# Kernel tuning notes

Measured on AMD Instinct MI355X. Metric: run time of the kernel, lower is better.

The kernel has to match this reference:

```python
import jax, jax.numpy as jnp
import numpy as np

B, L, D = 8, 64, 768
F, P, A = 50, 49, 49   # frames, patches, attention dim
N, C = 20000, 36       # grid points, grid_size**2 cells
LN_EPS = 1e-12


def setup_inputs() -> dict:
    key = jax.random.key(0)
    ks = jax.random.split(key, 16)
    s = 0.02
    return {
        "lang": jax.random.normal(ks[0], (B, L, D), jnp.float32),
        "lang_cls": jax.random.normal(ks[1], (B, A), jnp.float32),
        "frames": jax.random.normal(ks[2], (B, F, P, A), jnp.float32),
        "candidates": jax.random.normal(ks[3], (B, C, 2), jnp.float32),
        "grid_fts": jax.random.normal(ks[4], (B, N, D), jnp.float32),
        "grid_index": jax.random.randint(ks[5], (B, N), 0, C, jnp.int32),
        # SoftDotAttention params (bias=False in torch)
        "W_in": jax.random.normal(ks[6], (A, A), jnp.float32) * s,
        "W_out": jax.random.normal(ks[7], (A, 2 * A), jnp.float32) * s,
        # fc2: 49 -> demb
        "W_fc2": jax.random.normal(ks[8], (D, A), jnp.float32) * s,
        "b_fc2": jnp.zeros((D,), jnp.float32),
        # text_proj / grid_proj: 768 -> 768
        "W_text": jax.random.normal(ks[9], (D, D), jnp.float32) * s,
        "b_text": jnp.zeros((D,), jnp.float32),
        "W_grid": jax.random.normal(ks[10], (D, D), jnp.float32) * s,
        "b_grid": jnp.zeros((D,), jnp.float32),
        # candidate_encoder: Linear(2, demb) + LayerNorm(demb)
        "W_cand": jax.random.normal(ks[11], (D, 2), jnp.float32) * s,
        "b_cand": jnp.zeros((D,), jnp.float32),
        "ln_g": jnp.ones((D,), jnp.float32),
        "ln_b": jnp.zeros((D,), jnp.float32),
    }


def reference(lang, lang_cls, frames, candidates, grid_fts, grid_index,
              W_in, W_out, W_fc2, b_fc2, W_text, b_text, W_grid, b_grid,
              W_cand, b_cand, ln_g, ln_b):
    # ---- SoftDotAttention over every frame (vectorized over F) ----
    target = lang_cls @ W_in.T                                  # [B,A]
    attn = jnp.einsum('bfpa,ba->bfp', frames, target)           # [B,F,P]
    attn = jax.nn.softmax(attn, axis=-1)
    wctx = jnp.einsum('bfp,bfpa->bfa', attn, frames)            # [B,F,A]
    h = jnp.broadcast_to(lang_cls[:, None, :], wctx.shape)      # [B,F,A]
    att_frame = jnp.tanh(jnp.concatenate([wctx, h], -1) @ W_out.T)  # [B,F,A]
    emb_frames = att_frame @ W_fc2.T + b_fc2                    # [B,F,D]

    # ---- grid segment softmax-reduce ----
    text = lang @ W_text.T + b_text                             # [B,L,D]
    # score of each grid point = max over language tokens
    w = jnp.einsum('bnd,bld->bnl', grid_fts, text).max(-1)      # [B,N]
    g = grid_fts @ W_grid.T + b_grid                            # [B,N,D]
    mask = grid_index[..., None] == jnp.arange(C)[None, None]   # [B,N,C]
    logits = jnp.where(mask, w[..., None], -jnp.inf)            # [B,N,C]
    m = logits.max(axis=1, keepdims=True)                       # [B,1,C]
    m = jnp.where(jnp.isfinite(m), m, 0.0)
    e = jnp.where(mask, jnp.exp(logits - m), 0.0)
    den = e.sum(axis=1, keepdims=True)                          # [B,1,C]
    p = jnp.where(den > 0, e / jnp.maximum(den, 1e-30), 0.0)    # [B,N,C]
    grid_map = jnp.einsum('bnc,bnd->bcd', p, g)                 # [B,C,D]

    # ---- candidate encoder: Linear + LayerNorm, scaled by lang[:, :1, :] ----
    c = candidates @ W_cand.T + b_cand                          # [B,C,D]
    mu = c.mean(-1, keepdims=True)
    var = ((c - mu) ** 2).mean(-1, keepdims=True)
    c = (c - mu) * jax.lax.rsqrt(var + LN_EPS) * ln_g + ln_b
    emb_cand = c * lang[:, :1, :] + grid_map                    # [B,C,D]

    return jnp.concatenate([emb_frames, emb_cand], axis=1)      # [B,F+C,D]
```

## Files before the change

kernel.cpp:

```cpp
#include <hip/hip_runtime.h>
#include <math.h>

#define Bh 8
#define Lh 64
#define Dh 768
#define Fh 50
#define Ph 49
#define Ah 49
#define Nh 20000
#define Ch 36
#define CAP 2048
#define NCH 8
#define CUTE 2e-6f

typedef __bf16 bf16x8 __attribute__((ext_vector_type(8)));
typedef float f32x4 __attribute__((ext_vector_type(4)));
union U { uint4 u; bf16x8 v; };

__device__ __forceinline__ void cvt2(float a0, float a1, unsigned& h, unsigned& l) {
    unsigned u0 = __float_as_uint(a0), u1 = __float_as_uint(a1);
    unsigned h0 = u0 & 0xFFFF0000u, h1 = u1 & 0xFFFF0000u;
    h = (h0 >> 16) | h1;
    float l0 = a0 - __uint_as_float(h0);
    float l1 = a1 - __uint_as_float(h1);
    l = (__float_as_uint(l0) >> 16) | (__float_as_uint(l1) & 0xFFFF0000u);
}

__device__ __forceinline__ void cvt8(float4 p, float4 q, bf16x8& h8, bf16x8& l8) {
    U h, l;
    cvt2(p.x, p.y, h.u.x, l.u.x);
    cvt2(p.z, p.w, h.u.y, l.u.y);
    cvt2(q.x, q.y, h.u.z, l.u.z);
    cvt2(q.z, q.w, h.u.w, l.u.w);
    h8 = h.v; l8 = l.v;
}

__device__ __forceinline__ float dec_max(unsigned u) {
    if (u == 0u) return 0.f;
    return (u & 0x80000000u) ? __uint_as_float(u ^ 0x80000000u) : __uint_as_float(~u);
}

__global__ __launch_bounds__(256) void k_setup(const float* __restrict__ lang,
                                               const float* __restrict__ Wt,
                                               const float* __restrict__ bt,
                                               const float* __restrict__ frames,
                                               const float* __restrict__ lang_cls,
                                               const float* __restrict__ W_in,
                                               const float* __restrict__ W_out,
                                               const float* __restrict__ W_fc2,
                                               const float* __restrict__ b_fc2,
                                               uint4* __restrict__ textH,
                                               uint4* __restrict__ textL,
                                               unsigned* __restrict__ m_u,
                                               float* __restrict__ den,
                                               int* __restrict__ cnt,
                                               float* __restrict__ out) {
    __shared__ float smem[8 * Dh];
    int bx = blockIdx.x;
    int tid = threadIdx.x;

    if (bx < 64) {
        int b  = bx >> 3;
        int l0 = (bx & 7) * 8;
        float* ls = smem;
        for (int i = tid; i < 8 * Dh; i += 256)
            ls[i] = lang[((size_t)(b * Lh + l0 + i / Dh)) * Dh + (i % Dh)];
        __syncthreads();
        float acc[8][3];
#pragma unroll
        for (int li = 0; li < 8; ++li)
#pragma unroll
            for (int j = 0; j < 3; ++j) acc[li][j] = 0.f;
        for (int k = 0; k < Dh; k += 4) {
            float4 v[8];
#pragma unroll
            for (int li = 0; li < 8; ++li) v[li] = *(const float4*)&ls[li * Dh + k];
#pragma unroll
            for (int j = 0; j < 3; ++j) {
                int d = tid + j * 256;
                float4 wv = *(const float4*)&Wt[(size_t)d * Dh + k];
#pragma unroll
                for (int li = 0; li < 8; ++li)
                    acc[li][j] += wv.x * v[li].x + wv.y * v[li].y
                                + wv.z * v[li].z + wv.w * v[li].w;
            }
        }
        __syncthreads();
#pragma unroll
        for (int li = 0; li < 8; ++li)
#pragma unroll
            for (int j = 0; j < 3; ++j) {
                int d = tid + j * 256;
                ls[li * Dh + d] = acc[li][j] + bt[d];
            }
        __syncthreads();
        for (int i = tid; i < 768; i += 256) {
            int li = i / 96, idx = i % 96, ks = idx >> 2, j = idx & 3;
            int col = l0 + li, ct = col >> 4;
            const float* src = ls + li * Dh + ks * 32 + j * 8;
            U h, lo;
            cvt2(src[0], src[1], h.u.x, lo.u.x);
            cvt2(src[2], src[3], h.u.y, lo.u.y);
            cvt2(src[4], src[5], h.u.z, lo.u.z);
            cvt2(src[6], src[7], h.u.w, lo.u.w);
            int gid = ((b * 24 + ks) * 4 + ct) * 64 + (col & 15) + 16 * j;
            textH[gid] = h.u;
            textL[gid] = lo.u;
        }
    } else if (bx < 464) {
        int fid = bx - 64;
        int b = fid / Fh, f = fid % Fh;
        float* fr = smem;
        float* tg = smem + 2401;
        float* cl = smem + 2450;
        float* at = smem + 2499;
        float* wc = smem + 2548;
        float* af = smem + 2597;
        const float* fp = frames + ((size_t)(b * Fh + f)) * (Ph * Ah);
        for (int i = tid; i < Ph * Ah; i += 256) fr[i] = fp[i];
        if (tid < Ah) {
            cl[tid] = lang_cls[b * Ah + tid];
            float s = 0.f;
            for (int k = 0; k < Ah; ++k) s += lang_cls[b * Ah + k] * W_in[tid * Ah + k];
            tg[tid] = s;
        }
        __syncthreads();
        if (tid < Ph) {
            float s = 0.f;
            for (int a = 0; a < Ah; ++a) s += fr[tid * Ah + a] * tg[a];
            at[tid] = s;
        }
        __syncthreads();
        if (tid < 64) {
            float raw = (tid < Ph) ? at[tid] : -3.4e38f;
            float v = raw;
            for (int m = 32; m; m >>= 1) v = fmaxf(v, __shfl_xor(v, m));
            float e = (tid < Ph) ? expf(raw - v) : 0.f;
            float s = e;
            for (int m = 32; m; m >>= 1) s += __shfl_xor(s, m);
            if (tid < Ph) at[tid] = e / s;
        }
        __syncthreads();
        if (tid < Ah) {
            float s = 0.f;
            for (int p = 0; p < Ph; ++p) s += at[p] * fr[p * Ah + tid];
            wc[tid] = s;
        }
        __syncthreads();
        if (tid < Ah) {
            float s = 0.f;
            for (int a = 0; a < Ah; ++a)
                s += wc[a] * W_out[tid * (2 * Ah) + a] + cl[a] * W_out[tid * (2 * Ah) + Ah + a];
            af[tid] = tanhf(s);
        }
        __syncthreads();
        for (int d = tid; d < Dh; d += 256) {
            float s = b_fc2[d];
            for (int j = 0; j < Ah; ++j) s += af[j] * W_fc2[d * Ah + j];
            out[((size_t)(b * (Fh + Ch) + f)) * Dh + d] = s;
        }
    } else {
        for (int i = tid; i < Bh * Ch; i += 256) { m_u[i] = 0u; den[i] = 0.f; cnt[i] = 0; }
    }
}

__global__ __launch_bounds__(256) void k_wgf(const float* __restrict__ Wg,
                                             uint4* __restrict__ WgH,
                                             uint4* __restrict__ WgL) {
    int gid = blockIdx.x * 256 + threadIdx.x;
    int l = gid & 63;
    int rest = gid >> 6;
    int ct = rest % 48, ks = rest / 48;
    const float* src = Wg + (size_t)(ct * 16 + (l & 15)) * Dh + ks * 32 + (l >> 4) * 8;
    float4 p = *(const float4*)src;
    float4 q = *(const float4*)(src + 4);
    U h, lo;
    cvt2(p.x, p.y, h.u.x, lo.u.x);
    cvt2(p.z, p.w, h.u.y, lo.u.y);
    cvt2(q.x, q.y, h.u.z, lo.u.z);
    cvt2(q.z, q.w, h.u.w, lo.u.w);
    WgH[gid] = h.u;
    WgL[gid] = lo.u;
}

__global__ __launch_bounds__(256) void k_w(const float* __restrict__ grid,
                                           const uint4* __restrict__ textH,
                                           const uint4* __restrict__ textL,
                                           const int* __restrict__ gi,
                                           float* __restrict__ w,
                                           unsigned* __restrict__ m_u) {
    __shared__ float lds[2][4096];
    __shared__ unsigned mu[Ch];
    int b = blockIdx.y;
    int tid = threadIdx.x;
    int wv = tid >> 6, l = tid & 63;
    int n0 = blockIdx.x * 128;
    if (tid < Ch) mu[tid] = 0u;

    const float* gb = grid + (size_t)b * Nh * Dh;
    const uint4* pbh = textH + (size_t)b * 6144 + l;
    const uint4* pbl = textL + (size_t)b * 6144 + l;

    const float* srcA[4]; int dA[4];
#pragma unroll
    for (int r = 0; r < 4; ++r) {
        int s = r * 256 + tid, row = s >> 3, pos = s & 7;
        int rowg = n0 + row; if (rowg >= Nh) rowg = Nh - 1;
        srcA[r] = gb + (size_t)rowg * Dh + pos * 4;
        dA[r] = row * 32 + ((pos ^ (row & 7)) << 2);
    }
    int lm = l & 15, lh = l >> 4, r7 = lm & 7;
    int oA[2][2];
#pragma unroll
    for (int rt = 0; rt < 2; ++rt)
#pragma unroll
        for (int j = 0; j < 2; ++j)
            oA[rt][j] = (wv * 32 + rt * 16 + lm) * 32 + (((lh * 2 + j) ^ r7) << 2);

    {
        float4 v0 = *(const float4*)srcA[0];
        float4 v1 = *(const float4*)srcA[1];
        float4 v2 = *(const float4*)srcA[2];
        float4 v3 = *(const float4*)srcA[3];
        *(float4*)&lds[0][dA[0]] = v0;
        *(float4*)&lds[0][dA[1]] = v1;
        *(float4*)&lds[0][dA[2]] = v2;
        *(float4*)&lds[0][dA[3]] = v3;
    }
    __syncthreads();

    f32x4 acc[2][4];
#pragma unroll
    for (int i = 0; i < 2; ++i)
#pragma unroll
        for (int j = 0; j < 4; ++j) acc[i][j] = (f32x4){0.f, 0.f, 0.f, 0.f};

    for (int t = 0; t < 24; ++t) {
        int cur = t & 1;
        float4 p0, p1, p2, p3;
        bool pf = (t < 23);
        if (pf) {
            int o = (t + 1) * 32;
            p0 = *(const float4*)(srcA[0] + o);
            p1 = *(const float4*)(srcA[1] + o);
            p2 = *(const float4*)(srcA[2] + o);
            p3 = *(const float4*)(srcA[3] + o);
        }
        uint4 bh0 = pbh[t * 256 +   0], bh1 = pbh[t * 256 +  64];
        uint4 bh2 = pbh[t * 256 + 128], bh3 = pbh[t * 256 + 192];
        uint4 bl0 = pbl[t * 256 +   0], bl1 = pbl[t * 256 +  64];
        uint4 bl2 = pbl[t * 256 + 128], bl3 = pbl[t * 256 + 192];

        const float* L = lds[cur];
        float4 a00 = *(const float4*)&L[oA[0][0]];
        float4 a01 = *(const float4*)&L[oA[0][1]];
        float4 a10 = *(const float4*)&L[oA[1][0]];
        float4 a11 = *(const float4*)&L[oA[1][1]];
        bf16x8 ah0, al0, ah1, al1;
        cvt8(a00, a01, ah0, al0);
        cvt8(a10, a11, ah1, al1);

        uint4 bhu[4] = {bh0, bh1, bh2, bh3};
        uint4 blu[4] = {bl0, bl1, bl2, bl3};
#pragma unroll
        for (int ct = 0; ct < 4; ++ct) {
            U ubh, ubl; ubh.u = bhu[ct]; ubl.u = blu[ct];
            bf16x8 bh = ubh.v, bl = ubl.v;
            acc[0][ct] = __builtin_amdgcn_mfma_f32_16x16x32_bf16(ah0, bh, acc[0][ct], 0, 0, 0);
            acc[0][ct] = __builtin_amdgcn_mfma_f32_16x16x32_bf16(al0, bh, acc[0][ct], 0, 0, 0);
            acc[0][ct] = __builtin_amdgcn_mfma_f32_16x16x32_bf16(ah0, bl, acc[0][ct], 0, 0, 0);
            acc[1][ct] = __builtin_amdgcn_mfma_f32_16x16x32_bf16(ah1, bh, acc[1][ct], 0, 0, 0);
            acc[1][ct] = __builtin_amdgcn_mfma_f32_16x16x32_bf16(al1, bh, acc[1][ct], 0, 0, 0);
            acc[1][ct] = __builtin_amdgcn_mfma_f32_16x16x32_bf16(ah1, bl, acc[1][ct], 0, 0, 0);
        }
        if (pf) {
            float* D = lds[cur ^ 1];
            *(float4*)&D[dA[0]] = p0;
            *(float4*)&D[dA[1]] = p1;
            *(float4*)&D[dA[2]] = p2;
            *(float4*)&D[dA[3]] = p3;
        }
        __syncthreads();
    }

#pragma unroll
    for (int rt = 0; rt < 2; ++rt) {
        float m[4];
#pragma unroll
        for (int r = 0; r < 4; ++r) {
            m[r] = fmaxf(fmaxf(acc[rt][0][r], acc[rt][1][r]),
                         fmaxf(acc[rt][2][r], acc[rt][3][r]));
            m[r] = fmaxf(m[r], __shfl_xor(m[r], 1));
            m[r] = fmaxf(m[r], __shfl_xor(m[r], 2));
            m[r] = fmaxf(m[r], __shfl_xor(m[r], 4));
            m[r] = fmaxf(m[r], __shfl_xor(m[r], 8));
        }
        if (lm == 0) {
#pragma unroll
            for (int r = 0; r < 4; ++r) {
                int row = n0 + wv * 32 + rt * 16 + lh * 4 + r;
                if (row < Nh) {
                    w[b * Nh + row] = m[r];
                    unsigned u = __float_as_uint(m[r]);
                    u = (u & 0x80000000u) ? ~u : (u | 0x80000000u);
                    atomicMax(&mu[gi[b * Nh + row]], u);
                }
            }
        }
    }
    __syncthreads();
    if (tid < Ch && mu[tid]) atomicMax(&m_u[b * Ch + tid], mu[tid]);
}

__global__ __launch_bounds__(256) void k_epc(const float* __restrict__ w,
                                             const int* __restrict__ gi,
                                             const unsigned* __restrict__ m_u,
                                             float* __restrict__ den,
                                             int* __restrict__ cnt,
                                             int* __restrict__ bn,
                                             float* __restrict__ bp) {
    int b = blockIdx.y;
    int n = blockIdx.x * 256 + threadIdx.x;
    __shared__ float dn[Ch];
    if (threadIdx.x < Ch) dn[threadIdx.x] = 0.f;
    __syncthreads();
    if (n < Nh) {
        int c = gi[b * Nh + n];
        float e = expf(w[b * Nh + n] - dec_max(m_u[b * Ch + c]));
        atomicAdd(&dn[c], e);
        if (e > CUTE) {
            int pos = atomicAdd(&cnt[b * Ch + c], 1);
            if (pos < CAP) {
                bn[(b * Ch + c) * CAP + pos] = n;
                bp[(b * Ch + c) * CAP + pos] = e;
            }
        }
    }
    __syncthreads();
    if (threadIdx.x < Ch && dn[threadIdx.x] != 0.f)
        atomicAdd(&den[b * Ch + threadIdx.x], dn[threadIdx.x]);
}

__global__ __launch_bounds__(256) void k_S3(const float* __restrict__ grid,
                                            const int* __restrict__ cnt,
                                            const int* __restrict__ bn,
                                            const float* __restrict__ bp,
                                            float* __restrict__ Spart) {
    int c = blockIdx.x, dq = blockIdx.y;
    int b = blockIdx.z >> 3, ch = blockIdx.z & 7;
    int d = dq * 256 + threadIdx.x;
    int len = cnt[b * Ch + c]; if (len > CAP) len = CAP;
    int i0 = ch * (CAP / NCH);
    int i1 = i0 + (CAP / NCH); if (i1 > len) i1 = len;
    size_t base = (size_t)(b * Ch + c) * CAP;
    size_t po = ((size_t)(b * Ch + c) * NCH + ch) * Dh + d;
    const float* gb = grid + (size_t)b * Nh * Dh + d;
    float a[8] = {0.f, 0.f, 0.f, 0.f, 0.f, 0.f, 0.f, 0.f};
    int i = i0;
    for (; i + 8 <= i1; i += 8) {
        int nn[8]; float pp[8];
#pragma unroll
        for (int j = 0; j < 8; ++j) { nn[j] = bn[base + i + j]; pp[j] = bp[base + i + j]; }
#pragma unroll
        for (int j = 0; j < 8; ++j) a[j] += pp[j] * gb[(size_t)nn[j] * Dh];
    }
    for (; i < i1; ++i) a[0] += bp[base + i] * gb[(size_t)bn[base + i] * Dh];
    Spart[po] = ((a[0] + a[1]) + (a[2] + a[3])) + ((a[4] + a[5]) + (a[6] + a[7]));
}

__global__ __launch_bounds__(256) void k_red(const float* __restrict__ Spart,
                                             float* __restrict__ S) {
    int bc = blockIdx.x, dq = blockIdx.y;
    int d = dq * 256 + threadIdx.x;
    float s = 0.f;
#pragma unroll
    for (int ch = 0; ch < NCH; ++ch)
        s += Spart[((size_t)bc * NCH + ch) * Dh + d];
    S[(size_t)bc * Dh + d] = s;
}

__global__ __launch_bounds__(256) void k_gg2(const float* __restrict__ S,
                                             const float* __restrict__ den,
                                             const uint4* __restrict__ WgH,
                                             const uint4* __restrict__ WgL,
                                             const float* __restrict__ bg,
                                             float* __restrict__ G) {
    __shared__ float lds[2][4096];
    int tid = threadIdx.x;
    int wv = tid >> 6, l = tid & 63;
    int m0 = blockIdx.y * 128;
    int dt = blockIdx.x;

    const uint4* pbh = WgH + (size_t)dt * 256 + l;
    const uint4* pbl = WgL + (size_t)dt * 256 + l;

    const float* srcA[4]; int dA[4];
#pragma unroll
    for (int r = 0; r < 4; ++r) {
        int s = r * 256 + tid, row = s >> 3, pos = s & 7;
        int rowg = m0 + row; if (rowg >= Bh * Ch) rowg = Bh * Ch - 1;
        srcA[r] = S + (size_t)rowg * Dh + pos * 4;
        dA[r] = row * 32 + ((pos ^ (row & 7)) << 2);
    }
    int lm = l & 15, lh = l >> 4, r7 = lm & 7;
    int oA[2][2];
#pragma unroll
    for (int rt = 0; rt < 2; ++rt)
#pragma unroll
        for (int j = 0; j < 2; ++j)
            oA[rt][j] = (wv * 32 + rt * 16 + lm) * 32 + (((lh * 2 + j) ^ r7) << 2);

    {
        float4 v0 = *(const float4*)srcA[0];
        float4 v1 = *(const float4*)srcA[1];
        float4 v2 = *(const float4*)srcA[2];
        float4 v3 = *(const float4*)srcA[3];
        *(float4*)&lds[0][dA[0]] = v0;
        *(float4*)&lds[0][dA[1]] = v1;
        *(float4*)&lds[0][dA[2]] = v2;
        *(float4*)&lds[0][dA[3]] = v3;
    }
    __syncthreads();

    f32x4 acc[2][4];
#pragma unroll
    for (int i = 0; i < 2; ++i)
#pragma unroll
        for (int j = 0; j < 4; ++j) acc[i][j] = (f32x4){0.f, 0.f, 0.f, 0.f};

    for (int t = 0; t < 24; ++t) {
        int cur = t & 1;
        float4 p0, p1, p2, p3;
        bool pf = (t < 23);
        if (pf) {
            int o = (t + 1) * 32;
            p0 = *(const float4*)(srcA[0] + o);
            p1 = *(const float4*)(srcA[1] + o);
            p2 = *(const float4*)(srcA[2] + o);
            p3 = *(const float4*)(srcA[3] + o);
        }
        uint4 bh0 = pbh[t * 3072 +   0], bh1 = pbh[t * 3072 +  64];
        uint4 bh2 = pbh[t * 3072 + 128], bh3 = pbh[t * 3072 + 192];
        uint4 bl0 = pbl[t * 3072 +   0], bl1 = pbl[t * 3072 +  64];
        uint4 bl2 = pbl[t * 3072 + 128], bl3 = pbl[t * 3072 + 192];

        const float* L = lds[cur];
        float4 a00 = *(const float4*)&L[oA[0][0]];
        float4 a01 = *(const float4*)&L[oA[0][1]];
        float4 a10 = *(const float4*)&L[oA[1][0]];
        float4 a11 = *(const float4*)&L[oA[1][1]];
        bf16x8 ah0, al0, ah1, al1;
        cvt8(a00, a01, ah0, al0);
        cvt8(a10, a11, ah1, al1);

        uint4 bhu[4] = {bh0, bh1, bh2, bh3};
        uint4 blu[4] = {bl0, bl1, bl2, bl3};
#pragma unroll
        for (int ct = 0; ct < 4; ++ct) {
            U ubh, ubl; ubh.u = bhu[ct]; ubl.u = blu[ct];
            bf16x8 bh = ubh.v, bl = ubl.v;
            acc[0][ct] = __builtin_amdgcn_mfma_f32_16x16x32_bf16(ah0, bh, acc[0][ct], 0, 0, 0);
            acc[0][ct] = __builtin_amdgcn_mfma_f32_16x16x32_bf16(al0, bh, acc[0][ct], 0, 0, 0);
            acc[0][ct] = __builtin_amdgcn_mfma_f32_16x16x32_bf16(ah0, bl, acc[0][ct], 0, 0, 0);
            acc[1][ct] = __builtin_amdgcn_mfma_f32_16x16x32_bf16(ah1, bh, acc[1][ct], 0, 0, 0);
            acc[1][ct] = __builtin_amdgcn_mfma_f32_16x16x32_bf16(al1, bh, acc[1][ct], 0, 0, 0);
            acc[1][ct] = __builtin_amdgcn_mfma_f32_16x16x32_bf16(ah1, bl, acc[1][ct], 0, 0, 0);
        }
        if (pf) {
            float* D = lds[cur ^ 1];
            *(float4*)&D[dA[0]] = p0;
            *(float4*)&D[dA[1]] = p1;
            *(float4*)&D[dA[2]] = p2;
            *(float4*)&D[dA[3]] = p3;
        }
        __syncthreads();
    }

#pragma unroll
    for (int rt = 0; rt < 2; ++rt) {
#pragma unroll
        for (int r = 0; r < 4; ++r) {
            int row = m0 + wv * 32 + rt * 16 + lh * 4 + r;
            if (row < Bh * Ch) {
                float dv = den[row];
                float inv = (dv > 0.f) ? 1.f / dv : 0.f;
#pragma unroll
                for (int ct = 0; ct < 4; ++ct) {
                    int d = dt * 64 + ct * 16 + lm;
                    G[(size_t)row * Dh + d] = acc[rt][ct][r] * inv + bg[d];
                }
            }
        }
    }
}

__global__ __launch_bounds__(256) void k_final(const float* __restrict__ G,
                                               const float* __restrict__ den,
                                               const float* __restrict__ cands,
                                               const float* __restrict__ W_cand,
                                               const float* __restrict__ b_cand,
                                               const float* __restrict__ ln_g,
                                               const float* __restrict__ ln_b,
                                               const float* __restrict__ lang,
                                               float* __restrict__ out) {
    int b = blockIdx.x / Ch, c = blockIdx.x % Ch;
    int tid = threadIdx.x;
    __shared__ float cv[Dh];
    __shared__ float red[8];
    __shared__ float mu_s, rs_s;
    float cx = cands[(b * Ch + c) * 2 + 0], cy = cands[(b * Ch + c) * 2 + 1];
    for (int d = tid; d < Dh; d += 256)
        cv[d] = W_cand[d * 2] * cx + W_cand[d * 2 + 1] * cy + b_cand[d];
    __syncthreads();
    float ls = 0.f;
    for (int d = tid; d < Dh; d += 256) ls += cv[d];
    for (int m = 32; m; m >>= 1) ls += __shfl_xor(ls, m);
    if ((tid & 63) == 0) red[tid >> 6] = ls;
    __syncthreads();
    if (tid == 0) mu_s = (red[0] + red[1] + red[2] + red[3]) * (1.f / Dh);
    __syncthreads();
    float mu = mu_s;
    float lv = 0.f;
    for (int d = tid; d < Dh; d += 256) { float t = cv[d] - mu; lv += t * t; }
    for (int m = 32; m; m >>= 1) lv += __shfl_xor(lv, m);
    if ((tid & 63) == 0) red[4 + (tid >> 6)] = lv;
    __syncthreads();
    if (tid == 0) rs_s = rsqrtf((red[4] + red[5] + red[6] + red[7]) * (1.f / Dh) + 1e-12f);
    __syncthreads();
    float rs = rs_s;
    float dv = den[b * Ch + c];
#pragma unroll
    for (int j = 0; j < 3; ++j) {
        int d = tid + j * 256;
        float gm = (dv > 0.f) ? G[(size_t)(b * Ch + c) * Dh + d] : 0.f;
        float cn = (cv[d] - mu) * rs * ln_g[d] + ln_b[d];
        out[((size_t)(b * (Fh + Ch) + Fh + c)) * Dh + d] =
            cn * lang[((size_t)b * Lh) * Dh + d] + gm;
    }
}

extern "C" void kernel_launch(void* const* d_in, const int* in_sizes, int n_in,
                              void* d_out, int out_size, void* d_ws, size_t ws_size,
                              hipStream_t stream) {
    (void)in_sizes; (void)n_in; (void)out_size; (void)ws_size;
    const float* lang      = (const float*)d_in[0];
    const float* lang_cls  = (const float*)d_in[1];
    const float* frames    = (const float*)d_in[2];
    const float* cands     = (const float*)d_in[3];
    const float* grid_fts  = (const float*)d_in[4];
    const int*   grid_idx  = (const int*)d_in[5];
    const float* W_in      = (const float*)d_in[6];
    const float* W_out     = (const float*)d_in[7];
    const float* W_fc2     = (const float*)d_in[8];
    const float* b_fc2     = (const float*)d_in[9];
    const float* W_text    = (const float*)d_in[10];
    const float* b_text    = (const float*)d_in[11];
    const float* W_grid    = (const float*)d_in[12];
    const float* b_grid    = (const float*)d_in[13];
    const float* W_cand    = (const float*)d_in[14];
    const float* b_cand    = (const float*)d_in[15];
    const float* ln_g      = (const float*)d_in[16];
    const float* ln_b      = (const float*)d_in[17];
    float* out = (float*)d_out;
    float* ws  = (float*)d_ws;

    float*    wbuf  = ws;
    unsigned* m_u   = (unsigned*)(ws + 160000);
    float*    den   = ws + 160288;
    int*      cnt   = (int*)(ws + 160576);
    int*      bn    = (int*)(ws + 160864);
    float*    bp    = ws + 750688;
    float*    Spart = ws + 1340512;
    float*    G     = ws + 3109984;
    uint4*    textH = (uint4*)(ws + 3331168);
    uint4*    textL = (uint4*)(ws + 3527776);
    float*    S     = ws + 3724384;
    uint4*    WgH   = (uint4*)(ws + 3945568);
    uint4*    WgL   = (uint4*)(ws + 4240480);

    hipLaunchKernelGGL(k_setup,  dim3(465), dim3(256), 0, stream,
                       lang, W_text, b_text, frames, lang_cls, W_in, W_out, W_fc2, b_fc2,
                       textH, textL, m_u, den, cnt, out);
    hipLaunchKernelGGL(k_wgf,    dim3(288), dim3(256), 0, stream, W_grid, WgH, WgL);
    hipLaunchKernelGGL(k_w,      dim3((Nh + 127) / 128, Bh), dim3(256), 0, stream,
                       grid_fts, textH, textL, grid_idx, wbuf, m_u);
    hipLaunchKernelGGL(k_epc,    dim3(79, Bh), dim3(256), 0, stream,
                       wbuf, grid_idx, m_u, den, cnt, bn, bp);
    hipLaunchKernelGGL(k_S3,     dim3(Ch, 3, Bh * NCH), dim3(256), 0, stream,
                       grid_fts, cnt, bn, bp, Spart);
    hipLaunchKernelGGL(k_red,    dim3(Bh * Ch, 3), dim3(256), 0, stream, Spart, S);
    hipLaunchKernelGGL(k_gg2,    dim3(12, 3), dim3(256), 0, stream,
                       S, den, WgH, WgL, b_grid, G);
    hipLaunchKernelGGL(k_final,  dim3(Bh * Ch), dim3(256), 0, stream,
                       G, den, cands, W_cand, b_cand, ln_g, ln_b, lang, out);
}
```

Measured before the change: 282.2 us.

## Compute text projection with split-bf16 MFMA and transpose fc2 weights for coalescing

The scalar FP32 text_proj GEMM inside the setup kernel becomes a double-buffered MFMA GEMM using a hi/lo bf16 split for both operands, with W_text pre-split in a new prep kernel. The text fragment packing moves into a separate kernel. W_fc2 is transposed once so the frame-embedding loop reads coalesced memory. The aim is to shorten the setup stage, which was bound by scalar FP32 FMAs, at the cost of an extra kernel launch and more workspace traffic.

New measurement: 226.3 us, median of 2. 19.8% less time.

```diff
diff --git a/kernel.cpp b/kernel.cpp
--- a/kernel.cpp
+++ b/kernel.cpp
@@ -40,75 +40,162 @@
     return (u & 0x80000000u) ? __uint_as_float(u ^ 0x80000000u) : __uint_as_float(~u);
 }
 
-__global__ __launch_bounds__(256) void k_setup(const float* __restrict__ lang,
-                                               const float* __restrict__ Wt,
-                                               const float* __restrict__ bt,
-                                               const float* __restrict__ frames,
-                                               const float* __restrict__ lang_cls,
-                                               const float* __restrict__ W_in,
-                                               const float* __restrict__ W_out,
-                                               const float* __restrict__ W_fc2,
-                                               const float* __restrict__ b_fc2,
-                                               uint4* __restrict__ textH,
-                                               uint4* __restrict__ textL,
-                                               unsigned* __restrict__ m_u,
-                                               float* __restrict__ den,
-                                               int* __restrict__ cnt,
-                                               float* __restrict__ out) {
-    __shared__ float smem[8 * Dh];
+__global__ __launch_bounds__(256) void k_prep(const float* __restrict__ Wg,
+                                              const float* __restrict__ Wt,
+                                              const float* __restrict__ Wf2,
+                                              uint4* __restrict__ WgH, uint4* __restrict__ WgL,
+                                              uint4* __restrict__ WtH, uint4* __restrict__ WtL,
+                                              float* __restrict__ Wf2T,
+                                              unsigned* __restrict__ m_u,
+                                              float* __restrict__ den,
+                                              int* __restrict__ cnt) {
+    int bx = blockIdx.x, tid = threadIdx.x;
+    if (bx < 576) {
+        bool g = bx < 288;
+        int gid = (g ? bx : bx - 288) * 256 + tid;
+        const float* W = g ? Wg : Wt;
+        int l = gid & 63;
+        int rest = gid >> 6;
+        int ct = rest % 48, ks = rest / 48;
+        const float* src = W + (size_t)(ct * 16 + (l & 15)) * Dh + ks * 32 + (l >> 4) * 8;
+        float4 p = *(const float4*)src;
+        float4 q = *(const float4*)(src + 4);
+        U h, lo;
+        cvt2(p.x, p.y, h.u.x, lo.u.x);
+        cvt2(p.z, p.w, h.u.y, lo.u.y);
+        cvt2(q.x, q.y, h.u.z, lo.u.z);
+        cvt2(q.z, q.w, h.u.w, lo.u.w);
+        if (g) { WgH[gid] = h.u; WgL[gid] = lo.u; }
+        else   { WtH[gid] = h.u; WtL[gid] = lo.u; }
+    } else if (bx < 723) {
+        int i = (bx - 576) * 256 + tid;
+        int d = i / 49, j = i - d * 49;
+        Wf2T[j * Dh + d] = Wf2[i];
+    } else {
+        for (int i = tid; i < Bh * Ch; i += 256) { m_u[i] = 0u; den[i] = 0.f; cnt[i] = 0; }
+    }
+}
+
+__global__ __launch_bounds__(256) void k_tf(const float* __restrict__ lang,
+                                            const uint4* __restrict__ WtH,
+                                            const uint4* __restrict__ WtL,
+                                            const float* __restrict__ bt,
+                                            const float* __restrict__ frames,
+                                            const float* __restrict__ lang_cls,
+                                            const float* __restrict__ W_in,
+                                            const float* __restrict__ W_out,
+                                            const float* __restrict__ Wf2T,
+                                            const float* __restrict__ b_fc2,
+                                            float* __restrict__ text,
+                                            float* __restrict__ out) {
+    __shared__ float smem[8192];
     int bx = blockIdx.x;
     int tid = threadIdx.x;
 
-    if (bx < 64) {
-        int b  = bx >> 3;
-        int l0 = (bx & 7) * 8;
-        float* ls = smem;
-        for (int i = tid; i < 8 * Dh; i += 256)
-            ls[i] = lang[((size_t)(b * Lh + l0 + i / Dh)) * Dh + (i % Dh)];
-        __syncthreads();
-        float acc[8][3];
-#pragma unroll
-        for (int li = 0; li < 8; ++li)
-#pragma unroll
-            for (int j = 0; j < 3; ++j) acc[li][j] = 0.f;
-        for (int k = 0; k < Dh; k += 4) {
-            float4 v[8];
-#pragma unroll
-            for (int li = 0; li < 8; ++li) v[li] = *(const float4*)&ls[li * Dh + k];
-#pragma unroll
-            for (int j = 0; j < 3; ++j) {
-                int d = tid + j * 256;
-                float4 wv = *(const float4*)&Wt[(size_t)d * Dh + k];
-#pragma unroll
-                for (int li = 0; li < 8; ++li)
-                    acc[li][j] += wv.x * v[li].x + wv.y * v[li].y
-                                + wv.z * v[li].z + wv.w * v[li].w;
+    if (bx < 48) {
+        float (*lds)[4096] = (float(*)[4096])smem;
+        int wv = tid >> 6, l = tid & 63;
+        int dt = bx % 12;
+        int m0 = (bx / 12) * 128;
+
+        const uint4* pbh = WtH + (size_t)dt * 256 + l;
+        const uint4* pbl = WtL + (size_t)dt * 256 + l;
+
+        const float* srcA[4]; int dA[4];
+#pragma unroll
+        for (int r = 0; r < 4; ++r) {
+            int s = r * 256 + tid, row = s >> 3, pos = s & 7;
+            srcA[r] = lang + (size_t)(m0 + row) * Dh + pos * 4;
+            dA[r] = row * 32 + ((pos ^ (row & 7)) << 2);
+        }
+        int lm = l & 15, lh = l >> 4, r7 = lm & 7;
+        int oA[2][2];
+#pragma unroll
+        for (int rt = 0; rt < 2; ++rt)
+#pragma unroll
+            for (int j = 0; j < 2; ++j)
+                oA[rt][j] = (wv * 32 + rt * 16 + lm) * 32 + (((lh * 2 + j) ^ r7) << 2);
+
+        {
+            float4 v0 = *(const float4*)srcA[0];
+            float4 v1 = *(const float4*)srcA[1];
+            float4 v2 = *(const float4*)srcA[2];
+            float4 v3 = *(const float4*)srcA[3];
+            *(float4*)&lds[0][dA[0]] = v0;
+            *(float4*)&lds[0][dA[1]] = v1;
+            *(float4*)&lds[0][dA[2]] = v2;
+            *(float4*)&lds[0][dA[3]] = v3;
+        }
+        __syncthreads();
+
+        f32x4 acc[2][4];
+#pragma unroll
+        for (int i = 0; i < 2; ++i)
+#pragma unroll
+            for (int j = 0; j < 4; ++j) acc[i][j] = (f32x4){0.f, 0.f, 0.f, 0.f};
+
+        for (int t = 0; t < 24; ++t) {
+            int cur = t & 1;
+            float4 p0, p1, p2, p3;
+            bool pf = (t < 23);
+            if (pf) {
+                int o = (t + 1) * 32;
+                p0 = *(const float4*)(srcA[0] + o);
+                p1 = *(const float4*)(srcA[1] + o);
+                p2 = *(const float4*)(srcA[2] + o);
+                p3 = *(const float4*)(srcA[3] + o);
             }
-        }
-        __syncthreads();
-#pragma unroll
-        for (int li = 0; li < 8; ++li)
-#pragma unroll
-            for (int j = 0; j < 3; ++j) {
-                int d = tid + j * 256;
-                ls[li * Dh + d] = acc[li][j] + bt[d];
+            uint4 bh0 = pbh[t * 3072 +   0], bh1 = pbh[t * 3072 +  64];
+            uint4 bh2 = pbh[t * 3072 + 128], bh3 = pbh[t * 3072 + 192];
+            uint4 bl0 = pbl[t * 3072 +   0], bl1 = pbl[t * 3072 +  64];
+            uint4 bl2 = pbl[t * 3072 + 128], bl3 = pbl[t * 3072 + 192];
+
+            const float* L = lds[cur];
+            float4 a00 = *(const float4*)&L[oA[0][0]];
+            float4 a01 = *(const float4*)&L[oA[0][1]];
+            float4 a10 = *(const float4*)&L[oA[1][0]];
+            float4 a11 = *(const float4*)&L[oA[1][1]];
+            bf16x8 ah0, al0, ah1, al1;
+            cvt8(a00, a01, ah0, al0);
+            cvt8(a10, a11, ah1, al1);
+
+            uint4 bhu[4] = {bh0, bh1, bh2, bh3};
+            uint4 blu[4] = {bl0, bl1, bl2, bl3};
+#pragma unroll
+            for (int ct = 0; ct < 4; ++ct) {
+                U ubh, ubl; ubh.u = bhu[ct]; ubl.u = blu[ct];
+                bf16x8 bh = ubh.v, bl = ubl.v;
+                acc[0][ct] = __builtin_amdgcn_mfma_f32_16x16x32_bf16(ah0, bh, acc[0][ct], 0, 0, 0);
+                acc[0][ct] = __builtin_amdgcn_mfma_f32_16x16x32_bf16(al0, bh, acc[0][ct], 0, 0, 0);
+                acc[0][ct] = __builtin_amdgcn_mfma_f32_16x16x32_bf16(ah0, bl, acc[0][ct], 0, 0, 0);
+                acc[1][ct] = __builtin_amdgcn_mfma_f32_16x16x32_bf16(ah1, bh, acc[1][ct], 0, 0, 0);
+                acc[1][ct] = __builtin_amdgcn_mfma_f32_16x16x32_bf16(al1, bh, acc[1][ct], 0, 0, 0);
+                acc[1][ct] = __builtin_amdgcn_mfma_f32_16x16x32_bf16(ah1, bl, acc[1][ct], 0, 0, 0);
             }
-        __syncthreads();
-        for (int i = tid; i < 768; i += 256) {
-            int li = i / 96, idx = i % 96, ks = idx >> 2, j = idx & 3;
-            int col = l0 + li, ct = col >> 4;
-            const float* src = ls + li * Dh + ks * 32 + j * 8;
-            U h, lo;
-            cvt2(src[0], src[1], h.u.x, lo.u.x);
-            cvt2(src[2], src[3], h.u.y, lo.u.y);
-            cvt2(src[4], src[5], h.u.z, lo.u.z);
-            cvt2(src[6], src[7], h.u.w, lo.u.w);
-            int gid = ((b * 24 + ks) * 4 + ct) * 64 + (col & 15) + 16 * j;
-            textH[gid] = h.u;
-            textL[gid] = lo.u;
-        }
-    } else if (bx < 464) {
-        int fid = bx - 64;
+            if (pf) {
+                float* D = lds[cur ^ 1];
+                *(float4*)&D[dA[0]] = p0;
+                *(float4*)&D[dA[1]] = p1;
+                *(float4*)&D[dA[2]] = p2;
+                *(float4*)&D[dA[3]] = p3;
+            }
+            __syncthreads();
+        }
+
+#pragma unroll
+        for (int rt = 0; rt < 2; ++rt) {
+#pragma unroll
+            for (int r = 0; r < 4; ++r) {
+                int row = m0 + wv * 32 + rt * 16 + lh * 4 + r;
+#pragma unroll
+                for (int ct = 0; ct < 4; ++ct) {
+                    int d = dt * 64 + ct * 16 + lm;
+                    text[(size_t)row * Dh + d] = acc[rt][ct][r] + bt[d];
+                }
+            }
+        }
+    } else {
+        int fid = bx - 48;
         int b = fid / Fh, f = fid % Fh;
         float* fr = smem;
         float* tg = smem + 2401;
@@ -156,22 +243,22 @@
         __syncthreads();
         for (int d = tid; d < Dh; d += 256) {
             float s = b_fc2[d];
-            for (int j = 0; j < Ah; ++j) s += af[j] * W_fc2[d * Ah + j];
+            for (int j = 0; j < Ah; ++j) s += af[j] * Wf2T[j * Dh + d];
             out[((size_t)(b * (Fh + Ch) + f)) * Dh + d] = s;
         }
-    } else {
-        for (int i = tid; i < Bh * Ch; i += 256) { m_u[i] = 0u; den[i] = 0.f; cnt[i] = 0; }
-    }
-}
-
-__global__ __launch_bounds__(256) void k_wgf(const float* __restrict__ Wg,
-                                             uint4* __restrict__ WgH,
-                                             uint4* __restrict__ WgL) {
+    }
+}
+
+__global__ __launch_bounds__(256) void k_tfrag(const float* __restrict__ text,
+                                               uint4* __restrict__ textH,
+                                               uint4* __restrict__ textL) {
     int gid = blockIdx.x * 256 + threadIdx.x;
-    int l = gid & 63;
-    int rest = gid >> 6;
-    int ct = rest % 48, ks = rest / 48;
-    const float* src = Wg + (size_t)(ct * 16 + (l & 15)) * Dh + ks * 32 + (l >> 4) * 8;
+    int l  = gid & 63;
+    int ct = (gid >> 6) & 3;
+    int bk = gid >> 8;
+    int b  = bk / 24, ks = bk % 24;
+    const float* src = text + ((size_t)(b * Lh + ct * 16 + (l & 15))) * Dh
+                     + ks * 32 + (l >> 4) * 8;
     float4 p = *(const float4*)src;
     float4 q = *(const float4*)(src + 4);
     U h, lo;
@@ -179,8 +266,8 @@
     cvt2(p.z, p.w, h.u.y, lo.u.y);
     cvt2(q.x, q.y, h.u.z, lo.u.z);
     cvt2(q.z, q.w, h.u.w, lo.u.w);
-    WgH[gid] = h.u;
-    WgL[gid] = lo.u;
+    textH[gid] = h.u;
+    textL[gid] = lo.u;
 }
 
 __global__ __launch_bounds__(256) void k_w(const float* __restrict__ grid,
@@ -577,11 +664,17 @@
     float*    S     = ws + 3724384;
     uint4*    WgH   = (uint4*)(ws + 3945568);
     uint4*    WgL   = (uint4*)(ws + 4240480);
-
-    hipLaunchKernelGGL(k_setup,  dim3(465), dim3(256), 0, stream,
-                       lang, W_text, b_text, frames, lang_cls, W_in, W_out, W_fc2, b_fc2,
-                       textH, textL, m_u, den, cnt, out);
-    hipLaunchKernelGGL(k_wgf,    dim3(288), dim3(256), 0, stream, W_grid, WgH, WgL);
+    uint4*    WtH   = (uint4*)(ws + 4535392);
+    uint4*    WtL   = (uint4*)(ws + 4830304);
+    float*    Wf2T  = ws + 5125216;
+    float*    text  = ws + 5162848;
+
+    hipLaunchKernelGGL(k_prep,   dim3(724), dim3(256), 0, stream,
+                       W_grid, W_text, W_fc2, WgH, WgL, WtH, WtL, Wf2T, m_u, den, cnt);
+    hipLaunchKernelGGL(k_tf,     dim3(448), dim3(256), 0, stream,
+                       lang, WtH, WtL, b_text, frames, lang_cls, W_in, W_out, Wf2T, b_fc2,
+                       text, out);
+    hipLaunchKernelGGL(k_tfrag,  dim3(192), dim3(256), 0, stream, text, textH, textL);
     hipLaunchKernelGGL(k_w,      dim3((Nh + 127) / 128, Bh), dim3(256), 0, stream,
                        grid_fts, textH, textL, grid_idx, wbuf, m_u);
     hipLaunchKernelGGL(k_epc,    dim3(79, Bh), dim3(256), 0, stream,
```
